# Performance work log

Measured on AMD Instinct MI355X. Metric: run time of the kernel, lower is better.

The kernel has to match this reference:

```python
import jax, jax.numpy as jnp
import numpy as np

EMBED_DIM = 1024
NUM_HEADS = 16
L, N = 2048, 2


def setup_inputs() -> dict:
    key = jax.random.key(0)
    ks = jax.random.split(key, 7)
    E = EMBED_DIM
    inp = {
        "query": jax.random.normal(ks[0], (L, N, E), dtype=jnp.float32),
        "key": jax.random.normal(ks[1], (L, N, E), dtype=jnp.float32),
        "value": jax.random.normal(ks[2], (L, N, E), dtype=jnp.float32),
        "in_proj_weight": jax.random.normal(ks[3], (3 * E, E), dtype=jnp.float32) * (1.0 / np.sqrt(E)),
        "in_proj_bias": jnp.zeros((3 * E,), dtype=jnp.float32),
        "out_proj_weight": jax.random.normal(ks[4], (E, E), dtype=jnp.float32) * (1.0 / np.sqrt(E)),
        "out_proj_bias": jnp.zeros((E,), dtype=jnp.float32),
    }
    return inp


def reference(query, key, value, in_proj_weight, in_proj_bias, out_proj_weight, out_proj_bias):
    # query: (L, N, E); key/value: (S, N, E) -- seq-first like torch MHA
    Lq, Nb, E = query.shape
    H = NUM_HEADS
    hd = E // H
    scaling = float(hd) ** -0.5

    Wq, Wk, Wv = in_proj_weight[:E], in_proj_weight[E:2 * E], in_proj_weight[2 * E:]
    bq, bk, bv = in_proj_bias[:E], in_proj_bias[E:2 * E], in_proj_bias[2 * E:]

    q = (query @ Wq.T + bq) * scaling          # (L, N, E)
    k = key @ Wk.T + bk                         # (S, N, E)
    v = value @ Wv.T + bv                       # (S, N, E)

    S = k.shape[0]
    q = q.reshape(Lq, Nb, H, hd)
    k = k.reshape(S, Nb, H, hd)
    v = v.reshape(S, Nb, H, hd)

    # unfused MHA: materialize full (N, H, L, S) scores, softmax, weighted sum
    scores = jnp.einsum("lnhd,snhd->nhls", q, k)
    attn = jax.nn.softmax(scores, axis=-1)
    out = jnp.einsum("nhls,snhd->lnhd", attn, v).reshape(Lq, Nb, E)

    attn_output = out @ out_proj_weight.T + out_proj_bias  # (L, N, E)
    return attn_output
```

## Files before the change

### kernel.cpp

```cpp
#include <hip/hip_runtime.h>
#include <hip/hip_bf16.h>

typedef __attribute__((ext_vector_type(8))) short bf16x8;
typedef __attribute__((ext_vector_type(16))) float f32x16;
typedef __attribute__((ext_vector_type(4))) float f32x4;
typedef __attribute__((ext_vector_type(4))) short short4v;

#define MFMA16(a, b, c) __builtin_amdgcn_mfma_f32_16x16x32_bf16(a, b, c, 0, 0, 0)
#define MFMA32(a, b, c) __builtin_amdgcn_mfma_f32_32x32x16_bf16(a, b, c, 0, 0, 0)

constexpr float kQScale = 0.18033688011112042f;

__device__ __forceinline__ short f2bf(float f) {
  union { float f; unsigned u; } x; x.f = f;
  unsigned r = x.u + 0x7fffu + ((x.u >> 16) & 1u);
  return (short)(r >> 16);
}

__device__ __forceinline__ unsigned pk2(float a, float b) {
  __hip_bfloat162 h = __float22bfloat162_rn(make_float2(a, b));
  union { __hip_bfloat162 h; unsigned u; } c; c.h = h;
  return c.u;
}

__device__ __forceinline__ float fast_exp2(float x) {
  float r; asm("v_exp_f32 %0, %1" : "=v"(r) : "v"(x)); return r;
}

__device__ __forceinline__ void ld16(void* lds, const void* g) {
  __builtin_amdgcn_global_load_lds((const __attribute__((address_space(1))) void*)g,
                                   (__attribute__((address_space(3))) void*)lds, 16, 0, 0);
}

__global__ void conv_all(const float* __restrict__ q, const float* __restrict__ k,
                         const float* __restrict__ v, const float* __restrict__ w_in,
                         const float* __restrict__ w_out, short* __restrict__ X,
                         short* __restrict__ W) {
  int i = blockIdx.x * 256 + threadIdx.x;
  float4 val;
  float s = 1.0f;
  short* dst;
  if (i < 3145728) {
    int r = i >> 20, off = i & 0xFFFFF;
    const float* src = (r == 0) ? q : (r == 1) ? k : v;
    val = ((const float4*)src)[off];
    dst = X + (size_t)i * 4;
  } else {
    int j = i - 3145728;
    if (j < 786432) { val = ((const float4*)w_in)[j]; if (j < 262144) s = kQScale; }
    else            { val = ((const float4*)w_out)[j - 786432]; }
    dst = W + (size_t)j * 4;
  }
  short4v o;
  o.x = f2bf(val.x * s); o.y = f2bf(val.y * s); o.z = f2bf(val.z * s); o.w = f2bf(val.w * s);
  *(short4v*)dst = o;
}

template <int MODE>
__global__ __launch_bounds__(256) void gemm_nt(
    const short* __restrict__ A, const short* __restrict__ B,
    const float* __restrict__ bias, float* __restrict__ fout,
    short* __restrict__ q_ws, short* __restrict__ k_ws, short* __restrict__ vt_ws) {
  const int K = 1024;
  __shared__ __align__(16) short As[4096];
  __shared__ __align__(16) short Bs[4096];
  int tid = threadIdx.x;
  int w = tid >> 6, lane = tid & 63, g = lane >> 4, ln = lane & 15;
  int wr = w >> 1, wc = w & 1;

  int n0, m0;
  const short* Ab = A;
  if (MODE == 0) {
    int fid = blockIdx.x;
    int n_sub = fid / 96;
    int r = fid % 96;
    int z = r >> 5, m = r & 31;
    n0 = (z * 8 + n_sub) * 128;
    m0 = m * 128;
    Ab = A + (size_t)z * (4096u * 1024u);
  } else {
    int fid = blockIdx.x;
    n0 = (fid >> 5) * 128;
    m0 = (fid & 31) * 128;
  }

  int srow = w * 16 + (lane >> 2);
  int sch = (lane & 3) ^ ((srow >> 1) & 3);
  const short* ag0 = Ab + (size_t)(m0 + srow) * K + sch * 8;
  const short* ag1 = ag0 + (size_t)64 * K;
  const short* bg0 = B + (size_t)(n0 + srow) * K + sch * 8;
  const short* bg1 = bg0 + (size_t)64 * K;
  short* asd = As + w * 512;
  short* bsd = Bs + w * 512;

  f32x4 acc[4][4];
#pragma unroll
  for (int i = 0; i < 4; ++i)
#pragma unroll
    for (int j = 0; j < 4; ++j) acc[i][j] = (f32x4){0.f, 0.f, 0.f, 0.f};

  int rsw = (ln >> 1) & 3;
  for (int kb = 0; kb < K; kb += 32) {
    __syncthreads();
    ld16(asd,        ag0 + kb);
    ld16(asd + 2048, ag1 + kb);
    ld16(bsd,        bg0 + kb);
    ld16(bsd + 2048, bg1 + kb);
    __syncthreads();
    bf16x8 af[4], bfr[4];
#pragma unroll
    for (int fm = 0; fm < 4; ++fm)
      af[fm] = *(const bf16x8*)&As[(wr * 64 + fm * 16 + ln) * 32 + (g ^ rsw) * 8];
#pragma unroll
    for (int fn = 0; fn < 4; ++fn)
      bfr[fn] = *(const bf16x8*)&Bs[(wc * 64 + fn * 16 + ln) * 32 + (g ^ rsw) * 8];
#pragma unroll
    for (int fm = 0; fm < 4; ++fm)
#pragma unroll
      for (int fn = 0; fn < 4; ++fn) acc[fm][fn] = MFMA16(af[fm], bfr[fn], acc[fm][fn]);
  }

#pragma unroll
  for (int fm = 0; fm < 4; ++fm) {
#pragma unroll
    for (int fn = 0; fn < 4; ++fn) {
      int col = n0 + wc * 64 + fn * 16 + ln;
#pragma unroll
      for (int i = 0; i < 4; ++i) {
        int m = m0 + wr * 64 + fm * 16 + g * 4 + i;
        float val = acc[fm][fn][i];
        if (MODE == 1) {
          fout[(size_t)m * 1024 + col] = val + bias[col];
        } else {
          int z = col >> 10;
          int oe = col & 1023;
          float bval = bias[col];
          if (z == 0) bval *= kQScale;
          short bv = f2bf(val + bval);
          int hh = oe >> 6, d = oe & 63;
          int l = m >> 1, nb = m & 1;
          int nh = nb * 16 + hh;
          if (z == 0)      q_ws[((size_t)nh * 2048 + l) * 64 + d] = bv;
          else if (z == 1) k_ws[((size_t)nh * 2048 + l) * 64 + d] = bv;
          else {
            int u = l & 15;
            int lp = (l & ~15) | (u & 3) | ((u & 4) << 1) | ((u & 8) >> 1);
            vt_ws[((size_t)nh * 64 + d) * 2048 + lp] = bv;
          }
        }
      }
    }
  }
}

struct AttnCtx {
  const char* kg; const char* vg;
  char* klB; char* vlB;
  char* kdst; char* vdst;
  int lq, hi, swq;
  float lr;
};

__device__ __forceinline__ void attn_iter(
    int t, int& ksl, AttnCtx& c,
    f32x16& sCA, f32x16& sCB, f32x16& sNA, f32x16& sNB,
    f32x16 (&accO)[2], const bf16x8 (&qf)[4]) {
  if (t <= 28) {
    ld16(c.kdst + ksl * 8192,        c.kg);
    ld16(c.kdst + ksl * 8192 + 4096, c.kg + 4096);
    c.kg += 8192;
  }
  if (t <= 29) {
    int vs = ksl + 2; if (vs >= 3) vs -= 3;
    ld16(c.vdst + vs * 8192,        c.vg);
    ld16(c.vdst + vs * 8192 + 4096, c.vg + 131072);
    c.vg += 128;
  }

  if (t < 31) {
    int kr = ksl == 2 ? 0 : ksl + 1;
    const char* Kt = c.klB + kr * 8192;
#pragma unroll
    for (int i = 0; i < 16; ++i) { sNA[i] = 0.f; sNB[i] = 0.f; }
    __builtin_amdgcn_s_setprio(1);
#pragma unroll
    for (int kd = 0; kd < 4; ++kd) {
      int x = (32 * kd + 16 * c.hi) ^ c.swq;
      bf16x8 k0 = *(const bf16x8*)(Kt + c.lq * 128 + x);
      bf16x8 k1 = *(const bf16x8*)(Kt + (32 + c.lq) * 128 + x);
      sNA = MFMA32(k0, qf[kd], sNA);
      sNB = MFMA32(k1, qf[kd], sNB);
    }
    __builtin_amdgcn_s_setprio(0);
  }

#pragma unroll
  for (int i = 0; i < 16; ++i) { sCA[i] = fast_exp2(sCA[i]); sCB[i] = fast_exp2(sCB[i]); }
  float a0 = 0.f, a1 = 0.f, a2 = 0.f, a3 = 0.f;
#pragma unroll
  for (int i = 0; i < 4; ++i) {
    a0 += sCA[4 * i] + sCB[4 * i];
    a1 += sCA[4 * i + 1] + sCB[4 * i + 1];
    a2 += sCA[4 * i + 2] + sCB[4 * i + 2];
    a3 += sCA[4 * i + 3] + sCB[4 * i + 3];
  }
  c.lr += (a0 + a1) + (a2 + a3);

  bf16x8 pf[2][2];
  union PU { unsigned u[4]; bf16x8 v; };
#pragma unroll
  for (int ks = 0; ks < 2; ++ks) {
    PU a, b;
#pragma unroll
    for (int i = 0; i < 4; ++i) {
      a.u[i] = pk2(sCA[ks * 8 + 2 * i], sCA[ks * 8 + 2 * i + 1]);
      b.u[i] = pk2(sCB[ks * 8 + 2 * i], sCB[ks * 8 + 2 * i + 1]);
    }
    pf[0][ks] = a.v;
    pf[1][ks] = b.v;
  }

  const char* Vtl = c.vlB + ksl * 8192;
  __builtin_amdgcn_s_setprio(1);
#pragma unroll
  for (int dblk = 0; dblk < 2; ++dblk) {
    const char* vrow = Vtl + (dblk * 32 + c.lq) * 128;
#pragma unroll
    for (int sblk = 0; sblk < 2; ++sblk) {
#pragma unroll
      for (int ks = 0; ks < 2; ++ks) {
        bf16x8 vf = *(const bf16x8*)(vrow + ((sblk * 64 + ks * 32 + c.hi * 16) ^ c.swq));
        accO[dblk] = MFMA32(vf, pf[sblk][ks], accO[dblk]);
      }
    }
  }
  __builtin_amdgcn_s_setprio(0);

  if (t < 29)       asm volatile("s_waitcnt vmcnt(4)" ::: "memory");
  else if (t == 29) asm volatile("s_waitcnt vmcnt(2)" ::: "memory");
  else if (t == 30) asm volatile("s_waitcnt vmcnt(0)" ::: "memory");
  if (t < 31) __builtin_amdgcn_s_barrier();

  ksl = ksl == 2 ? 0 : ksl + 1;
}

__global__ __launch_bounds__(256, 2) void attn5(const short* __restrict__ Qws,
                                                const short* __restrict__ Kws,
                                                const short* __restrict__ Vt,
                                                short* __restrict__ Ows) {
  const int L = 2048;
  int bid = blockIdx.x;
  int nh = bid & 31, qt = bid >> 5;
  int nb = nh >> 4, h = nh & 15;
  int tid = threadIdx.x;
  int w = tid >> 6, lane = tid & 63;
  int lq = lane & 31, hi = lane >> 5;

  __shared__ __align__(16) char Kl[3][8192];
  __shared__ __align__(16) char Vl[3][8192];

  int q0 = qt * 128 + w * 32;
  const short* Qb = Qws + (size_t)nh * L * 64;
  const char* Kb = (const char*)(Kws + (size_t)nh * L * 64);
  const char* Vb = (const char*)(Vt + (size_t)nh * 64 * L);

  bf16x8 qf[4];
#pragma unroll
  for (int kd = 0; kd < 4; ++kd)
    qf[kd] = *(const bf16x8*)(Qb + (size_t)(q0 + lq) * 64 + kd * 16 + hi * 8);

  int rA = tid >> 3, cc = (tid & 7) * 16;
  int swr = (rA & 7) << 4;

  AttnCtx c;
  c.kg = Kb + rA * 128 + (cc ^ swr);
  c.vg = Vb + rA * 4096 + (cc ^ swr);
  c.klB = (char*)&Kl[0][0];
  c.vlB = (char*)&Vl[0][0];
  c.kdst = c.klB + w * 1024;
  c.vdst = c.vlB + w * 1024;
  c.lq = lq; c.hi = hi; c.swq = (lq & 7) << 4;
  c.lr = 0.f;

  ld16(c.kdst,                c.kg);
  ld16(c.kdst + 4096,         c.kg + 4096);
  ld16(c.kdst + 8192,         c.kg + 8192);
  ld16(c.kdst + 8192 + 4096,  c.kg + 8192 + 4096);
  ld16(c.vdst,                c.vg);
  ld16(c.vdst + 4096,         c.vg + 131072);
  ld16(c.kdst + 16384,        c.kg + 16384);
  ld16(c.kdst + 16384 + 4096, c.kg + 16384 + 4096);
  ld16(c.vdst + 8192,         c.vg + 128);
  ld16(c.vdst + 8192 + 4096,  c.vg + 128 + 131072);
  c.kg += 3 * 8192;
  c.vg += 2 * 128;

  f32x16 accO[2];
#pragma unroll
  for (int i = 0; i < 16; ++i) { accO[0][i] = 0.f; accO[1][i] = 0.f; }
  f32x16 s0A, s0B, s1A, s1B;

  asm volatile("s_waitcnt vmcnt(4)" ::: "memory");
  __builtin_amdgcn_s_barrier();

#pragma unroll
  for (int i = 0; i < 16; ++i) { s0A[i] = 0.f; s0B[i] = 0.f; }
  __builtin_amdgcn_s_setprio(1);
#pragma unroll
  for (int kd = 0; kd < 4; ++kd) {
    int x = (32 * kd + 16 * hi) ^ c.swq;
    bf16x8 k0 = *(const bf16x8*)(c.klB + lq * 128 + x);
    bf16x8 k1 = *(const bf16x8*)(c.klB + (32 + lq) * 128 + x);
    s0A = MFMA32(k0, qf[kd], s0A);
    s0B = MFMA32(k1, qf[kd], s0B);
  }
  __builtin_amdgcn_s_setprio(0);

  __builtin_amdgcn_s_barrier();

  int ksl = 0;
  for (int it = 0; it < 16; ++it) {
    attn_iter(2 * it,     ksl, c, s0A, s0B, s1A, s1B, accO, qf);
    attn_iter(2 * it + 1, ksl, c, s1A, s1B, s0A, s0B, accO, qf);
  }

  float lr = c.lr + __shfl_xor(c.lr, 32);
  float inv = 1.0f / lr;
  int qrow = q0 + lq;
  short* orow = Ows + (size_t)(qrow * 2 + nb) * 1024 + h * 64;
#pragma unroll
  for (int dblk = 0; dblk < 2; ++dblk) {
#pragma unroll
    for (int grp = 0; grp < 4; ++grp) {
      short4v o;
      o.x = f2bf(accO[dblk][grp * 4 + 0] * inv);
      o.y = f2bf(accO[dblk][grp * 4 + 1] * inv);
      o.z = f2bf(accO[dblk][grp * 4 + 2] * inv);
      o.w = f2bf(accO[dblk][grp * 4 + 3] * inv);
      *(short4v*)(orow + dblk * 32 + grp * 8 + hi * 4) = o;
    }
  }
}

extern "C" void kernel_launch(void* const* d_in, const int* in_sizes, int n_in,
                              void* d_out, int out_size, void* d_ws, size_t ws_size,
                              hipStream_t stream) {
  const float* q     = (const float*)d_in[0];
  const float* k     = (const float*)d_in[1];
  const float* v     = (const float*)d_in[2];
  const float* w_in  = (const float*)d_in[3];
  const float* b_in  = (const float*)d_in[4];
  const float* w_out = (const float*)d_in[5];
  const float* b_out = (const float*)d_in[6];
  float* out = (float*)d_out;
  char* ws = (char*)d_ws;

  short* X    = (short*)(ws);
  short* Wio  = (short*)(ws + 25165824);
  short* Wout = (short*)(ws + 31457280);
  short* Qws  = (short*)(ws + 33554432);
  short* Kws  = (short*)(ws + 41943040);
  short* Vt   = (short*)(ws + 50331648);
  short* Ows  = (short*)(ws + 58720256);

  conv_all<<<16384, 256, 0, stream>>>(q, k, v, w_in, w_out, X, Wio);
  gemm_nt<0><<<768, 256, 0, stream>>>(X, Wio, b_in, nullptr, Qws, Kws, Vt);
  attn5<<<512, 256, 0, stream>>>(Qws, Kws, Vt, Ows);
  gemm_nt<1><<<256, 256, 0, stream>>>(Ows, Wout, b_out, out, nullptr, nullptr, nullptr);
}
```

Measured before the change: 129.1 us.

## Triple-buffer GEMM shared-memory tiles with async prefetch and vmcnt waits

The projection GEMM now keeps three LDS stages and issues global-to-LDS loads two K-steps ahead. It waits on partial vmcnt with one barrier per iteration, replacing the two full syncthreads per iteration. It also raises wave priority around the MFMA block. The aim is to hide global load latency behind matrix math, at the cost of triple the LDS (48KB) and therefore possibly lower occupancy. Correctness depends on ld16 being a direct-to-LDS load counted by vmcnt and on a single barrier being enough to avoid overwriting a slot that is still being read.

```diff
diff --git a/kernel.cpp b/kernel.cpp
--- a/kernel.cpp
+++ b/kernel.cpp
@@ -62,8 +62,9 @@
     const float* __restrict__ bias, float* __restrict__ fout,
     short* __restrict__ q_ws, short* __restrict__ k_ws, short* __restrict__ vt_ws) {
   const int K = 1024;
-  __shared__ __align__(16) short As[4096];
-  __shared__ __align__(16) short Bs[4096];
+  const int NT = K / 32;
+  __shared__ __align__(16) short As[3][4096];
+  __shared__ __align__(16) short Bs[3][4096];
   int tid = threadIdx.x;
   int w = tid >> 6, lane = tid & 63, g = lane >> 4, ln = lane & 15;
   int wr = w >> 1, wc = w & 1;
@@ -90,8 +91,15 @@
   const short* ag1 = ag0 + (size_t)64 * K;
   const short* bg0 = B + (size_t)(n0 + srow) * K + sch * 8;
   const short* bg1 = bg0 + (size_t)64 * K;
-  short* asd = As + w * 512;
-  short* bsd = Bs + w * 512;
+  const int sdo = w * 512;
+
+#define STAGE(s, kb)                        \
+  do {                                      \
+    ld16(&As[s][sdo],        ag0 + (kb));   \
+    ld16(&As[s][sdo + 2048], ag1 + (kb));   \
+    ld16(&Bs[s][sdo],        bg0 + (kb));   \
+    ld16(&Bs[s][sdo + 2048], bg1 + (kb));   \
+  } while (0)
 
   f32x4 acc[4][4];
 #pragma unroll
@@ -100,25 +108,40 @@
     for (int j = 0; j < 4; ++j) acc[i][j] = (f32x4){0.f, 0.f, 0.f, 0.f};
 
   int rsw = (ln >> 1) & 3;
-  for (int kb = 0; kb < K; kb += 32) {
-    __syncthreads();
-    ld16(asd,        ag0 + kb);
-    ld16(asd + 2048, ag1 + kb);
-    ld16(bsd,        bg0 + kb);
-    ld16(bsd + 2048, bg1 + kb);
-    __syncthreads();
+
+  STAGE(0, 0);
+  STAGE(1, 32);
+  asm volatile("s_waitcnt vmcnt(4)" ::: "memory");
+  __builtin_amdgcn_s_barrier();
+
+  int slot = 0;
+  for (int t = 0; t < NT; ++t) {
+    int kp = (t + 2) * 32;
+    int s2 = slot + 2; if (s2 >= 3) s2 -= 3;
+    if (kp < K) STAGE(s2, kp);
+
     bf16x8 af[4], bfr[4];
 #pragma unroll
     for (int fm = 0; fm < 4; ++fm)
-      af[fm] = *(const bf16x8*)&As[(wr * 64 + fm * 16 + ln) * 32 + (g ^ rsw) * 8];
+      af[fm] = *(const bf16x8*)&As[slot][(wr * 64 + fm * 16 + ln) * 32 + (g ^ rsw) * 8];
 #pragma unroll
     for (int fn = 0; fn < 4; ++fn)
-      bfr[fn] = *(const bf16x8*)&Bs[(wc * 64 + fn * 16 + ln) * 32 + (g ^ rsw) * 8];
+      bfr[fn] = *(const bf16x8*)&Bs[slot][(wc * 64 + fn * 16 + ln) * 32 + (g ^ rsw) * 8];
+    __builtin_amdgcn_s_setprio(1);
 #pragma unroll
     for (int fm = 0; fm < 4; ++fm)
 #pragma unroll
       for (int fn = 0; fn < 4; ++fn) acc[fm][fn] = MFMA16(af[fm], bfr[fn], acc[fm][fn]);
-  }
+    __builtin_amdgcn_s_setprio(0);
+
+    if (t + 1 < NT) {
+      if (kp < K) asm volatile("s_waitcnt vmcnt(4)" ::: "memory");
+      else        asm volatile("s_waitcnt vmcnt(0)" ::: "memory");
+      __builtin_amdgcn_s_barrier();
+    }
+    slot = slot == 2 ? 0 : slot + 1;
+  }
+#undef STAGE
 
 #pragma unroll
   for (int fm = 0; fm < 4; ++fm) {
```

Measured after the change: 133.5 us. +3.4%, slower.

## Use 256x256 triple-buffered pipelined tiles for QKV projection GEMM

Applied to the files above, without the earlier changes.

Replaces the 128x128 single-buffered QKV projection GEMM with a dedicated 512-thread kernel using 256x256 tiles and a three-stage LDS ring, prefetching two k-steps ahead with vmcnt waits and raised wave priority around the MFMA block. The aim is more reuse per loaded tile and overlap of global loads with compute instead of a sync-load-compute loop. The output GEMM is split into its own non-templated kernel with the bias load hoisted. The trade-off is that only 192 blocks launch, fewer than the CU count, and larger register and LDS use per block lowers occupancy.

```diff
diff --git a/kernel.cpp b/kernel.cpp
--- a/kernel.cpp
+++ b/kernel.cpp
@@ -56,11 +56,119 @@
   *(short4v*)dst = o;
 }
 
-template <int MODE>
-__global__ __launch_bounds__(256) void gemm_nt(
+__global__ __launch_bounds__(512, 2) void gemm256(
     const short* __restrict__ A, const short* __restrict__ B,
-    const float* __restrict__ bias, float* __restrict__ fout,
+    const float* __restrict__ bias,
     short* __restrict__ q_ws, short* __restrict__ k_ws, short* __restrict__ vt_ws) {
+  const int K = 1024;
+  __shared__ __align__(16) short As[3][8192];
+  __shared__ __align__(16) short Bs[3][8192];
+  int tid = threadIdx.x;
+  int w = tid >> 6, lane = tid & 63, g = lane >> 4, ln = lane & 15;
+  int wr = w >> 2, wc = w & 3;
+
+  int fid = blockIdx.x;
+  int n = fid / 48;
+  int r = fid % 48;
+  int z = r >> 4, m = r & 15;
+  int m0 = m * 256;
+  int n0 = z * 1024 + n * 256;
+  const short* Ab = A + (size_t)z * (4096u * 1024u);
+
+  int srow = tid >> 2;
+  int sch = (tid & 3) ^ ((srow >> 1) & 3);
+  const short* ag0 = Ab + (size_t)(m0 + srow) * K + sch * 8;
+  const short* ag1 = ag0 + (size_t)128 * K;
+  const short* bg0 = B + (size_t)(n0 + srow) * K + sch * 8;
+  const short* bg1 = bg0 + (size_t)128 * K;
+  char* asl = (char*)&As[0][0];
+  char* bsl = (char*)&Bs[0][0];
+  const int wb = w * 1024;
+
+#define STG(s, kb)                                      \
+  do {                                                  \
+    ld16(asl + (s) * 16384 + wb,        ag0 + (kb));    \
+    ld16(asl + (s) * 16384 + 8192 + wb, ag1 + (kb));    \
+    ld16(bsl + (s) * 16384 + wb,        bg0 + (kb));    \
+    ld16(bsl + (s) * 16384 + 8192 + wb, bg1 + (kb));    \
+  } while (0)
+
+  f32x4 acc[8][4];
+#pragma unroll
+  for (int i = 0; i < 8; ++i)
+#pragma unroll
+    for (int j = 0; j < 4; ++j) acc[i][j] = (f32x4){0.f, 0.f, 0.f, 0.f};
+
+  int rsw = (ln >> 1) & 3;
+
+  STG(0, 0);
+  STG(1, 32);
+  asm volatile("s_waitcnt vmcnt(4)" ::: "memory");
+  __builtin_amdgcn_s_barrier();
+
+  int slot = 0;
+  for (int t = 0; t < 32; ++t) {
+    int kp = (t + 2) * 32;
+    int s2 = slot + 2; if (s2 >= 3) s2 -= 3;
+    if (kp < K) STG(s2, kp);
+
+    bf16x8 af[8], bf[4];
+#pragma unroll
+    for (int fm = 0; fm < 8; ++fm)
+      af[fm] = *(const bf16x8*)(asl + slot * 16384 +
+                                (wr * 128 + fm * 16 + ln) * 64 + ((g ^ rsw) * 16));
+#pragma unroll
+    for (int fn = 0; fn < 4; ++fn)
+      bf[fn] = *(const bf16x8*)(bsl + slot * 16384 +
+                                (wc * 64 + fn * 16 + ln) * 64 + ((g ^ rsw) * 16));
+    __builtin_amdgcn_s_setprio(1);
+#pragma unroll
+    for (int fm = 0; fm < 8; ++fm)
+#pragma unroll
+      for (int fn = 0; fn < 4; ++fn) acc[fm][fn] = MFMA16(af[fm], bf[fn], acc[fm][fn]);
+    __builtin_amdgcn_s_setprio(0);
+
+    if (t < 31) {
+      if (kp < K) asm volatile("s_waitcnt vmcnt(4)" ::: "memory");
+      else        asm volatile("s_waitcnt vmcnt(0)" ::: "memory");
+      __builtin_amdgcn_s_barrier();
+    }
+    slot = slot == 2 ? 0 : slot + 1;
+  }
+#undef STG
+
+#pragma unroll
+  for (int fm = 0; fm < 8; ++fm) {
+#pragma unroll
+    for (int fn = 0; fn < 4; ++fn) {
+      int col = n0 + wc * 64 + fn * 16 + ln;
+      int zc = col >> 10;
+      int oe = col & 1023;
+      float bval = bias[col];
+      if (zc == 0) bval *= kQScale;
+      int hh = oe >> 6, d = oe & 63;
+      int nh_base = hh;
+#pragma unroll
+      for (int i = 0; i < 4; ++i) {
+        int mm = m0 + wr * 128 + fm * 16 + g * 4 + i;
+        short bv = f2bf(acc[fm][fn][i] + bval);
+        int l = mm >> 1, nb = mm & 1;
+        int nh = nb * 16 + nh_base;
+        if (zc == 0)      q_ws[((size_t)nh * 2048 + l) * 64 + d] = bv;
+        else if (zc == 1) k_ws[((size_t)nh * 2048 + l) * 64 + d] = bv;
+        else {
+          int u = l & 15;
+          int lp = (l & ~15) | (u & 3) | ((u & 4) << 1) | ((u & 8) >> 1);
+          vt_ws[((size_t)nh * 64 + d) * 2048 + lp] = bv;
+        }
+      }
+    }
+  }
+}
+
+__global__ __launch_bounds__(256) void gemm_out(
+    const short* __restrict__ A, const short* __restrict__ B,
+    const float* __restrict__ bias, float* __restrict__ fout) {
   const int K = 1024;
   __shared__ __align__(16) short As[4096];
   __shared__ __align__(16) short Bs[4096];
@@ -68,25 +176,13 @@
   int w = tid >> 6, lane = tid & 63, g = lane >> 4, ln = lane & 15;
   int wr = w >> 1, wc = w & 1;
 
-  int n0, m0;
-  const short* Ab = A;
-  if (MODE == 0) {
-    int fid = blockIdx.x;
-    int n_sub = fid / 96;
-    int r = fid % 96;
-    int z = r >> 5, m = r & 31;
-    n0 = (z * 8 + n_sub) * 128;
-    m0 = m * 128;
-    Ab = A + (size_t)z * (4096u * 1024u);
-  } else {
-    int fid = blockIdx.x;
-    n0 = (fid >> 5) * 128;
-    m0 = (fid & 31) * 128;
-  }
+  int fid = blockIdx.x;
+  int n0 = (fid >> 5) * 128;
+  int m0 = (fid & 31) * 128;
 
   int srow = w * 16 + (lane >> 2);
   int sch = (lane & 3) ^ ((srow >> 1) & 3);
-  const short* ag0 = Ab + (size_t)(m0 + srow) * K + sch * 8;
+  const short* ag0 = A + (size_t)(m0 + srow) * K + sch * 8;
   const short* ag1 = ag0 + (size_t)64 * K;
   const short* bg0 = B + (size_t)(n0 + srow) * K + sch * 8;
   const short* bg1 = bg0 + (size_t)64 * K;
@@ -125,29 +221,11 @@
 #pragma unroll
     for (int fn = 0; fn < 4; ++fn) {
       int col = n0 + wc * 64 + fn * 16 + ln;
+      float bval = bias[col];
 #pragma unroll
       for (int i = 0; i < 4; ++i) {
         int m = m0 + wr * 64 + fm * 16 + g * 4 + i;
-        float val = acc[fm][fn][i];
-        if (MODE == 1) {
-          fout[(size_t)m * 1024 + col] = val + bias[col];
-        } else {
-          int z = col >> 10;
-          int oe = col & 1023;
-          float bval = bias[col];
-          if (z == 0) bval *= kQScale;
-          short bv = f2bf(val + bval);
-          int hh = oe >> 6, d = oe & 63;
-          int l = m >> 1, nb = m & 1;
-          int nh = nb * 16 + hh;
-          if (z == 0)      q_ws[((size_t)nh * 2048 + l) * 64 + d] = bv;
-          else if (z == 1) k_ws[((size_t)nh * 2048 + l) * 64 + d] = bv;
-          else {
-            int u = l & 15;
-            int lp = (l & ~15) | (u & 3) | ((u & 4) << 1) | ((u & 8) >> 1);
-            vt_ws[((size_t)nh * 64 + d) * 2048 + lp] = bv;
-          }
-        }
+        fout[(size_t)m * 1024 + col] = acc[fm][fn][i] + bval;
       }
     }
   }
@@ -364,7 +442,7 @@
   short* Ows  = (short*)(ws + 58720256);
 
   conv_all<<<16384, 256, 0, stream>>>(q, k, v, w_in, w_out, X, Wio);
-  gemm_nt<0><<<768, 256, 0, stream>>>(X, Wio, b_in, nullptr, Qws, Kws, Vt);
+  gemm256<<<192, 512, 0, stream>>>(X, Wio, b_in, Qws, Kws, Vt);
   attn5<<<512, 256, 0, stream>>>(Qws, Kws, Vt, Ows);
-  gemm_nt<1><<<256, 256, 0, stream>>>(Ows, Wout, b_out, out, nullptr, nullptr, nullptr);
-}
+  gemm_out<<<256, 256, 0, stream>>>(Ows, Wout, b_out, out);
+}
```

Result: slower. 153.4 us (+18.8%).

## Shrink GEMM N-tile to 64 and loop over Q/K/V inside each block

Applied to the files above, without the earlier changes.

The projection GEMM changes its tile from 128x128 to 128x64 and makes each block handle all three Q/K/V sub-GEMMs in sequence, launching 512 blocks instead of 768. The output projection also uses 128x64 tiles, going from 256 to 512 blocks. The goal is better occupancy and a more even load across CUs: a smaller accumulator and less LDS per block, plus 512 blocks for the output GEMM. In exchange each block does less MFMA work per A-tile load, so the A operand is fetched twice as often across blocks, and each projection block now does three times as many serial K-loops.

```diff
diff --git a/kernel.cpp b/kernel.cpp
--- a/kernel.cpp
+++ b/kernel.cpp
@@ -57,95 +57,86 @@
 }
 
 template <int MODE>
-__global__ __launch_bounds__(256) void gemm_nt(
+__global__ __launch_bounds__(256) void gemm_z(
     const short* __restrict__ A, const short* __restrict__ B,
     const float* __restrict__ bias, float* __restrict__ fout,
     short* __restrict__ q_ws, short* __restrict__ k_ws, short* __restrict__ vt_ws) {
   const int K = 1024;
   __shared__ __align__(16) short As[4096];
-  __shared__ __align__(16) short Bs[4096];
+  __shared__ __align__(16) short Bs[2048];
   int tid = threadIdx.x;
   int w = tid >> 6, lane = tid & 63, g = lane >> 4, ln = lane & 15;
   int wr = w >> 1, wc = w & 1;
 
-  int n0, m0;
-  const short* Ab = A;
-  if (MODE == 0) {
-    int fid = blockIdx.x;
-    int n_sub = fid / 96;
-    int r = fid % 96;
-    int z = r >> 5, m = r & 31;
-    n0 = (z * 8 + n_sub) * 128;
-    m0 = m * 128;
-    Ab = A + (size_t)z * (4096u * 1024u);
-  } else {
-    int fid = blockIdx.x;
-    n0 = (fid >> 5) * 128;
-    m0 = (fid & 31) * 128;
-  }
+  int fid = blockIdx.x;
+  int mt = fid & 31, nt = fid >> 5;
+  int m0 = mt * 128;
 
   int srow = w * 16 + (lane >> 2);
   int sch = (lane & 3) ^ ((srow >> 1) & 3);
-  const short* ag0 = Ab + (size_t)(m0 + srow) * K + sch * 8;
-  const short* ag1 = ag0 + (size_t)64 * K;
-  const short* bg0 = B + (size_t)(n0 + srow) * K + sch * 8;
-  const short* bg1 = bg0 + (size_t)64 * K;
   short* asd = As + w * 512;
   short* bsd = Bs + w * 512;
-
-  f32x4 acc[4][4];
-#pragma unroll
-  for (int i = 0; i < 4; ++i)
-#pragma unroll
-    for (int j = 0; j < 4; ++j) acc[i][j] = (f32x4){0.f, 0.f, 0.f, 0.f};
-
   int rsw = (ln >> 1) & 3;
-  for (int kb = 0; kb < K; kb += 32) {
-    __syncthreads();
-    ld16(asd,        ag0 + kb);
-    ld16(asd + 2048, ag1 + kb);
-    ld16(bsd,        bg0 + kb);
-    ld16(bsd + 2048, bg1 + kb);
-    __syncthreads();
-    bf16x8 af[4], bfr[4];
-#pragma unroll
-    for (int fm = 0; fm < 4; ++fm)
-      af[fm] = *(const bf16x8*)&As[(wr * 64 + fm * 16 + ln) * 32 + (g ^ rsw) * 8];
-#pragma unroll
-    for (int fn = 0; fn < 4; ++fn)
-      bfr[fn] = *(const bf16x8*)&Bs[(wc * 64 + fn * 16 + ln) * 32 + (g ^ rsw) * 8];
-#pragma unroll
-    for (int fm = 0; fm < 4; ++fm)
-#pragma unroll
-      for (int fn = 0; fn < 4; ++fn) acc[fm][fn] = MFMA16(af[fm], bfr[fn], acc[fm][fn]);
-  }
-
-#pragma unroll
-  for (int fm = 0; fm < 4; ++fm) {
-#pragma unroll
-    for (int fn = 0; fn < 4; ++fn) {
-      int col = n0 + wc * 64 + fn * 16 + ln;
-#pragma unroll
-      for (int i = 0; i < 4; ++i) {
-        int m = m0 + wr * 64 + fm * 16 + g * 4 + i;
-        float val = acc[fm][fn][i];
-        if (MODE == 1) {
-          fout[(size_t)m * 1024 + col] = val + bias[col];
-        } else {
-          int z = col >> 10;
-          int oe = col & 1023;
-          float bval = bias[col];
-          if (z == 0) bval *= kQScale;
-          short bv = f2bf(val + bval);
-          int hh = oe >> 6, d = oe & 63;
-          int l = m >> 1, nb = m & 1;
-          int nh = nb * 16 + hh;
-          if (z == 0)      q_ws[((size_t)nh * 2048 + l) * 64 + d] = bv;
-          else if (z == 1) k_ws[((size_t)nh * 2048 + l) * 64 + d] = bv;
-          else {
-            int u = l & 15;
-            int lp = (l & ~15) | (u & 3) | ((u & 4) << 1) | ((u & 8) >> 1);
-            vt_ws[((size_t)nh * 64 + d) * 2048 + lp] = bv;
+
+  const int NZ = (MODE == 0) ? 3 : 1;
+  for (int z = 0; z < NZ; ++z) {
+    const short* Az = A + (size_t)z * (4096u * 1024u);
+    const short* ag0 = Az + (size_t)(m0 + srow) * K + sch * 8;
+    const short* ag1 = ag0 + (size_t)64 * K;
+    const short* bg0 = B + (size_t)(z * 1024 + nt * 64 + srow) * K + sch * 8;
+
+    f32x4 acc[4][2];
+#pragma unroll
+    for (int i = 0; i < 4; ++i)
+#pragma unroll
+      for (int j = 0; j < 2; ++j) acc[i][j] = (f32x4){0.f, 0.f, 0.f, 0.f};
+
+    for (int kb = 0; kb < K; kb += 32) {
+      __syncthreads();
+      ld16(asd,        ag0 + kb);
+      ld16(asd + 2048, ag1 + kb);
+      ld16(bsd,        bg0 + kb);
+      __syncthreads();
+      bf16x8 af[4], bfr[2];
+#pragma unroll
+      for (int fm = 0; fm < 4; ++fm)
+        af[fm] = *(const bf16x8*)&As[(wr * 64 + fm * 16 + ln) * 32 + (g ^ rsw) * 8];
+#pragma unroll
+      for (int fn = 0; fn < 2; ++fn)
+        bfr[fn] = *(const bf16x8*)&Bs[(wc * 32 + fn * 16 + ln) * 32 + (g ^ rsw) * 8];
+#pragma unroll
+      for (int fm = 0; fm < 4; ++fm)
+#pragma unroll
+        for (int fn = 0; fn < 2; ++fn) acc[fm][fn] = MFMA16(af[fm], bfr[fn], acc[fm][fn]);
+    }
+
+#pragma unroll
+    for (int fm = 0; fm < 4; ++fm) {
+#pragma unroll
+      for (int fn = 0; fn < 2; ++fn) {
+        int col = z * 1024 + nt * 64 + wc * 32 + fn * 16 + ln;
+#pragma unroll
+        for (int i = 0; i < 4; ++i) {
+          int m = m0 + wr * 64 + fm * 16 + g * 4 + i;
+          float val = acc[fm][fn][i];
+          if (MODE == 1) {
+            fout[(size_t)m * 1024 + col] = val + bias[col];
+          } else {
+            int zc = col >> 10;
+            int oe = col & 1023;
+            float bval = bias[col];
+            if (zc == 0) bval *= kQScale;
+            short bv = f2bf(val + bval);
+            int hh = oe >> 6, d = oe & 63;
+            int l = m >> 1, nb = m & 1;
+            int nh = nb * 16 + hh;
+            if (zc == 0)      q_ws[((size_t)nh * 2048 + l) * 64 + d] = bv;
+            else if (zc == 1) k_ws[((size_t)nh * 2048 + l) * 64 + d] = bv;
+            else {
+              int u = l & 15;
+              int lp = (l & ~15) | (u & 3) | ((u & 4) << 1) | ((u & 8) >> 1);
+              vt_ws[((size_t)nh * 64 + d) * 2048 + lp] = bv;
+            }
           }
         }
       }
@@ -364,7 +355,7 @@
   short* Ows  = (short*)(ws + 58720256);
 
   conv_all<<<16384, 256, 0, stream>>>(q, k, v, w_in, w_out, X, Wio);
-  gemm_nt<0><<<768, 256, 0, stream>>>(X, Wio, b_in, nullptr, Qws, Kws, Vt);
+  gemm_z<0><<<512, 256, 0, stream>>>(X, Wio, b_in, nullptr, Qws, Kws, Vt);
   attn5<<<512, 256, 0, stream>>>(Qws, Kws, Vt, Ows);
-  gemm_nt<1><<<256, 256, 0, stream>>>(Ows, Wout, b_out, out, nullptr, nullptr, nullptr);
-}
+  gemm_z<1><<<512, 256, 0, stream>>>(Ows, Wout, b_out, out, nullptr, nullptr, nullptr);
+}
```

After: 183.7 us. +42.2%, slower.
